# Kernel optimization log

Measured on AMD Instinct MI355X. Metric: run time of the kernel, lower is better.

The kernel has to match this reference:

```python
import jax, jax.numpy as jnp
import numpy as np

D_MODEL = 2048
N_HEADS = 16
N_KV_HEADS = 4
HEAD_DIM = D_MODEL // N_HEADS  # 128
N_REP = N_HEADS // N_KV_HEADS  # 4
ROPE_BASE = 10000.0


def _rope_tables(T, head_dim, dtype):
    inv_freq = 1.0 / (ROPE_BASE ** (jnp.arange(0, head_dim, 2, dtype=jnp.float32) / head_dim))
    t = jnp.arange(T, dtype=jnp.float32)
    freqs = jnp.outer(t, inv_freq)               # [T, hd/2]
    emb = jnp.concatenate([freqs, freqs], axis=-1)  # [T, hd]
    return jnp.cos(emb).astype(dtype), jnp.sin(emb).astype(dtype)


def _rotate_half(x):
    x1, x2 = jnp.split(x, 2, axis=-1)
    return jnp.concatenate([-x2, x1], axis=-1)


def _apply_rope(x, cos, sin):
    # x: [B, H, T, hd]; cos/sin: [T, hd]
    return x * cos[None, None] + _rotate_half(x) * sin[None, None]


def setup_inputs() -> dict:
    key = jax.random.key(0)
    ks = jax.random.split(key, 5)
    B, T = 2, 2048
    s_in = 1.0 / np.sqrt(D_MODEL)
    return {
        "x": jax.random.normal(ks[0], (B, T, D_MODEL), jnp.float32),
        "Wq": jax.random.normal(ks[1], (D_MODEL, D_MODEL), jnp.float32) * s_in,
        "Wk": jax.random.normal(ks[2], (D_MODEL, N_KV_HEADS * HEAD_DIM), jnp.float32) * s_in,
        "Wv": jax.random.normal(ks[3], (D_MODEL, N_KV_HEADS * HEAD_DIM), jnp.float32) * s_in,
        "Wo": jax.random.normal(ks[4], (D_MODEL, D_MODEL), jnp.float32) * s_in,
    }


def reference(x, Wq, Wk, Wv, Wo):
    B, T, C = x.shape
    scale = HEAD_DIM ** -0.5
    q = (x @ Wq).reshape(B, T, N_HEADS, HEAD_DIM).transpose(0, 2, 1, 3)     # [B,H,T,hd]
    k = (x @ Wk).reshape(B, T, N_KV_HEADS, HEAD_DIM).transpose(0, 2, 1, 3)  # [B,Hkv,T,hd]
    v = (x @ Wv).reshape(B, T, N_KV_HEADS, HEAD_DIM).transpose(0, 2, 1, 3)
    cos, sin = _rope_tables(T, HEAD_DIM, x.dtype)
    q = _apply_rope(q, cos, sin)
    k = _apply_rope(k, cos, sin)
    # GQA: group query heads; avoid materializing expanded K/V
    qg = q.reshape(B, N_KV_HEADS, N_REP, T, HEAD_DIM)
    scores = jnp.einsum('bgrtd,bgsd->bgrts', qg, k) * scale                 # [B,Hkv,rep,T,S]
    causal = jnp.tril(jnp.ones((T, T), dtype=bool))
    scores = jnp.where(causal[None, None, None], scores, jnp.finfo(scores.dtype).min)
    attn = jax.nn.softmax(scores, axis=-1)
    out = jnp.einsum('bgrts,bgsd->bgrtd', attn, v)                          # [B,Hkv,rep,T,hd]
    out = out.reshape(B, N_HEADS, T, HEAD_DIM).transpose(0, 2, 1, 3).reshape(B, T, C)
    return out @ Wo, k, v
```

## Files before the change

kernel.cpp:

```cpp
#include <hip/hip_runtime.h>
#include <hip/hip_bf16.h>
#include <type_traits>


typedef short  short8 __attribute__((ext_vector_type(8)));
typedef float  f32x4  __attribute__((ext_vector_type(4)));
typedef float  f32x16 __attribute__((ext_vector_type(16)));

#define AS1(p) ((__attribute__((address_space(1))) void*)(p))
#define AS3(p) ((__attribute__((address_space(3))) void*)(p))

static __device__ inline short bf_bits(float f) {
    __hip_bfloat16 h = __float2bfloat16(f);
    return *reinterpret_cast<short*>(&h);
}

__global__ __launch_bounds__(256) void convert_x_kernel(
    const float* __restrict__ x, __hip_bfloat16* __restrict__ xb)
{
    int i = (blockIdx.x * 256 + threadIdx.x) * 4;
    float4 v = *reinterpret_cast<const float4*>(x + i);
    ushort4 o;
    o.x = (unsigned short)bf_bits(v.x);
    o.y = (unsigned short)bf_bits(v.y);
    o.z = (unsigned short)bf_bits(v.z);
    o.w = (unsigned short)bf_bits(v.w);
    *reinterpret_cast<ushort4*>(reinterpret_cast<unsigned short*>(xb) + i) = o;
}

__global__ void transpose_all_kernel(
    const float* __restrict__ Wq, const float* __restrict__ Wk,
    const float* __restrict__ Wv, const float* __restrict__ Wo,
    __hip_bfloat16* __restrict__ WqkvT, __hip_bfloat16* __restrict__ WoT)
{
    __shared__ float tile[32][33];
    const int nb = blockIdx.x;
    const int k0 = blockIdx.y * 32;
    const int tx = threadIdx.x, ty = threadIdx.y;
    const float* W; int srcN, sn0, drow; __hip_bfloat16* dst;
    if (nb < 64) {
        int blk = nb & 3;
        int blk2 = ((blk & 1) << 1) | (blk >> 1);
        W = Wq; srcN = 2048; sn0 = nb * 32;
        dst = WqkvT; drow = ((nb >> 2) * 4 + blk2) * 32;
    } else if (nb < 80) {
        int i = nb - 64, blk = i & 3;
        int blk2 = ((blk & 1) << 1) | (blk >> 1);
        W = Wk; srcN = 512; sn0 = i * 32;
        dst = WqkvT; drow = 2048 + ((i >> 2) * 4 + blk2) * 32;
    } else if (nb < 96) {
        int i = nb - 80;
        W = Wv; srcN = 512; sn0 = i * 32;
        dst = WqkvT; drow = 2560 + i * 32;
    } else {
        int i = nb - 96;
        W = Wo; srcN = 2048; sn0 = i * 32;
        dst = WoT; drow = i * 32;
    }
#pragma unroll
    for (int i = 0; i < 32; i += 8)
        tile[ty + i][tx] = W[(size_t)(k0 + ty + i) * srcN + sn0 + tx];
    __syncthreads();
#pragma unroll
    for (int i = 0; i < 32; i += 8)
        dst[(size_t)(drow + ty + i) * 2048 + k0 + tx] = __float2bfloat16(tile[tx][ty + i]);
}

static __device__ inline void xcd_decode(int bid, int M, int N, int& m0, int& n0)
{
    const int xcd = bid & 7;
    const int idx = bid >> 3;
    const int mpx = (M >> 7) >> 3;
    const int rem = idx % (mpx * 4);
    const int mb = xcd * mpx + rem % mpx;
    const int nb = (idx / (mpx * 4)) * 4 + rem / mpx;
    m0 = mb << 7;
    n0 = nb << 7;
}

#define WAITV4 asm volatile("s_waitcnt vmcnt(4)" ::: "memory")
#define WAITV0 asm volatile("s_waitcnt vmcnt(0)" ::: "memory")

template <typename CT>
__global__ __launch_bounds__(256) void gemm_bt_kernel(
    const __hip_bfloat16* __restrict__ A,
    const __hip_bfloat16* __restrict__ BT,
    CT* __restrict__ C, int M, int N, int K)
{
    const int tid  = threadIdx.x;
    const int w    = tid >> 6;
    const int lane = tid & 63;
    const int l31  = lane & 31;
    const int hi   = lane >> 5;
    int m0, n0;
    xcd_decode(blockIdx.x, M, N, m0, n0);
    const int wm = (w >> 1) << 6;
    const int wn = (w & 1) << 6;

    __shared__ __hip_bfloat16 As[2][128 * 64];
    __shared__ __hip_bfloat16 Bs[2][128 * 64];

    f32x16 acc[2][2] = {};

#define GSTAGE(buf, k0_)                                                            \
    {                                                                               \
        _Pragma("unroll")                                                           \
        for (int i = 0; i < 4; ++i) {                                               \
            int c = tid + i * 256;                                                  \
            int row = c >> 3;                                                       \
            int soct = (c & 7) ^ (row & 7);                                         \
            const __hip_bfloat16* ga = A  + (size_t)(m0 + row) * K + (k0_) + soct * 8; \
            const __hip_bfloat16* gb = BT + (size_t)(n0 + row) * K + (k0_) + soct * 8; \
            __builtin_amdgcn_global_load_lds(AS1(ga), AS3(&As[buf][c * 8]), 16, 0, 0); \
            __builtin_amdgcn_global_load_lds(AS1(gb), AS3(&Bs[buf][c * 8]), 16, 0, 0); \
        }                                                                           \
    }

    GSTAGE(0, 0);
    __syncthreads();
    int cur = 0;
    const int nk = K >> 6;

    for (int t = 0; t < nk; ++t) {
        if (t + 1 < nk) GSTAGE(cur ^ 1, (t + 1) << 6);

#pragma unroll
        for (int ks = 0; ks < 4; ++ks) {
            const int oct = ((ks * 2 + hi) ^ (l31 & 7)) << 3;
            short8 a[2], b[2];
#pragma unroll
            for (int mi = 0; mi < 2; ++mi)
                a[mi] = *reinterpret_cast<const short8*>(
                    reinterpret_cast<const short*>(&As[cur][0]) + (wm + mi * 32 + l31) * 64 + oct);
#pragma unroll
            for (int ni = 0; ni < 2; ++ni)
                b[ni] = *reinterpret_cast<const short8*>(
                    reinterpret_cast<const short*>(&Bs[cur][0]) + (wn + ni * 32 + l31) * 64 + oct);
#pragma unroll
            for (int mi = 0; mi < 2; ++mi)
#pragma unroll
                for (int ni = 0; ni < 2; ++ni)
                    acc[mi][ni] = __builtin_amdgcn_mfma_f32_32x32x16_bf16(
                        a[mi], b[ni], acc[mi][ni], 0, 0, 0);
        }
        __syncthreads();
        cur ^= 1;
    }
#undef GSTAGE

#pragma unroll
    for (int mi = 0; mi < 2; ++mi)
#pragma unroll
        for (int ni = 0; ni < 2; ++ni)
#pragma unroll
            for (int reg = 0; reg < 16; ++reg) {
                int row = m0 + wm + mi * 32 + (reg & 3) + 8 * (reg >> 2) + 4 * hi;
                int col = n0 + wn + ni * 32 + l31;
                float v = acc[mi][ni][reg];
                if constexpr (std::is_same<CT, float>::value)
                    C[(size_t)row * N + col] = v;
                else
                    C[(size_t)row * N + col] = __float2bfloat16(v);
            }
}

__global__ __launch_bounds__(256) void gemm_qkv_fused(
    const __hip_bfloat16* __restrict__ A,
    const __hip_bfloat16* __restrict__ BT,
    __hip_bfloat16* __restrict__ qkv,
    float* __restrict__ outk,
    float* __restrict__ outv,
    __hip_bfloat16* __restrict__ VT)
{
    const int tid  = threadIdx.x;
    const int w    = tid >> 6;
    const int lane = tid & 63;
    const int l31  = lane & 31;
    const int hi   = lane >> 5;
    int m0, n0;
    xcd_decode(blockIdx.x, 4096, 3072, m0, n0);
    const int wm = (w >> 1) << 6;
    const int wn = (w & 1) << 6;
    const int K = 2048;

    __shared__ __hip_bfloat16 As[3][128 * 32];
    __shared__ __hip_bfloat16 Bs[3][128 * 32];

    f32x16 acc[2][2] = {};

#define GSTAGE(buf, k0_)                                                             \
    {                                                                                \
        _Pragma("unroll")                                                            \
        for (int i = 0; i < 2; ++i) {                                                \
            int c = tid + i * 256;                                                   \
            int row = c >> 2;                                                        \
            int soct = (c & 3) ^ ((row >> 1) & 3);                                   \
            const __hip_bfloat16* ga = A  + (size_t)(m0 + row) * K + (k0_) + soct * 8; \
            const __hip_bfloat16* gb = BT + (size_t)(n0 + row) * K + (k0_) + soct * 8; \
            __builtin_amdgcn_global_load_lds(AS1(ga), AS3(&As[buf][c * 8]), 16, 0, 0); \
            __builtin_amdgcn_global_load_lds(AS1(gb), AS3(&Bs[buf][c * 8]), 16, 0, 0); \
        }                                                                            \
    }

    const int nk = 64;
    GSTAGE(0, 0);
    GSTAGE(1, 32);
    int cur = 0, stg = 2;

    for (int t = 0; t < nk; ++t) {
        if (t == nk - 1) { WAITV0; } else { WAITV4; }
        __builtin_amdgcn_s_barrier();
        __builtin_amdgcn_sched_barrier(0);
        if (t + 2 < nk) GSTAGE(stg, (t + 2) << 5);

#pragma unroll
        for (int ks = 0; ks < 2; ++ks) {
            short8 a[2], b[2];
#pragma unroll
            for (int mi = 0; mi < 2; ++mi) {
                int row = wm + mi * 32 + l31;
                a[mi] = *reinterpret_cast<const short8*>(
                    reinterpret_cast<const short*>(&As[cur][0])
                    + row * 32 + (((ks * 2 + hi) ^ ((row >> 1) & 3)) << 3));
            }
#pragma unroll
            for (int ni = 0; ni < 2; ++ni) {
                int row = wn + ni * 32 + l31;
                b[ni] = *reinterpret_cast<const short8*>(
                    reinterpret_cast<const short*>(&Bs[cur][0])
                    + row * 32 + (((ks * 2 + hi) ^ ((row >> 1) & 3)) << 3));
            }
#pragma unroll
            for (int mi = 0; mi < 2; ++mi)
#pragma unroll
                for (int ni = 0; ni < 2; ++ni)
                    acc[mi][ni] = __builtin_amdgcn_mfma_f32_32x32x16_bf16(
                        a[mi], b[ni], acc[mi][ni], 0, 0, 0);
        }
        cur = (cur == 2) ? 0 : cur + 1;
        stg = (stg == 2) ? 0 : stg + 1;
    }
#undef GSTAGE

    const int hc = n0 >> 7;
    if (hc < 20) {
        const int c0 = wn + l31;
        const int d_lo = (wn ? 32 : 0) + l31;
        const float invf = exp2f((float)d_lo * -0.20762050593046f);
        const int kh = hc - 16;
#pragma unroll
        for (int mi = 0; mi < 2; ++mi)
#pragma unroll
            for (int reg = 0; reg < 16; ++reg) {
                int row = m0 + wm + mi * 32 + (reg & 3) + 8 * (reg >> 2) + 4 * hi;
                int b = row >> 11, t = row & 2047;
                float ang = (float)t * invf;
                float s = __sinf(ang), c = __cosf(ang);
                float x1 = acc[mi][0][reg], x2 = acc[mi][1][reg];
                float o1 = x1 * c - x2 * s;
                float o2 = x2 * c + x1 * s;
                __hip_bfloat16* q = qkv + (size_t)row * 3072 + hc * 128 + c0;
                q[0]  = __float2bfloat16(o1);
                q[32] = __float2bfloat16(o2);
                if (hc >= 16) {
                    float* ok = outk + (size_t)((b * 4 + kh) * 2048 + t) * 128 + d_lo;
                    ok[0]  = o1;
                    ok[64] = o2;
                }
            }
    } else {
        const int kh = hc - 20;
#pragma unroll
        for (int mi = 0; mi < 2; ++mi)
#pragma unroll
            for (int reg = 0; reg < 16; ++reg) {
                int row = m0 + wm + mi * 32 + (reg & 3) + 8 * (reg >> 2) + 4 * hi;
                int b = row >> 11, t = row & 2047;
#pragma unroll
                for (int ni = 0; ni < 2; ++ni) {
                    int d = wn + ni * 32 + l31;
                    float v = acc[mi][ni][reg];
                    outv[(size_t)((b * 4 + kh) * 2048 + t) * 128 + d] = v;
                    VT[(size_t)((b * 4 + kh) * 128 + d) * 2048 + t] = __float2bfloat16(v);
                }
            }
    }
}

__global__ __launch_bounds__(256, 2) void attn_kernel(
    const __hip_bfloat16* __restrict__ qkv,
    const __hip_bfloat16* __restrict__ VT,
    __hip_bfloat16* __restrict__ outO)
{
    const int bh = blockIdx.x;
    const int b = bh >> 4, h = bh & 15;
    const int kh = h >> 2;
    const int yb = blockIdx.y;
    const int qblk = (yb < 8) ? (15 - yb) : (yb - 8);
    const int tid = threadIdx.x;
    const int w = tid >> 6;
    const int lane = tid & 63;
    const int lo16 = lane & 15, grp = lane >> 4;
    const int qrow0 = qblk * 128 + w * 32;

    __shared__ short Ks[2][64 * 128];
    __shared__ short Vs[2][128 * 64];
    __shared__ short Ps[4][32 * 64];

    const short* qkvs = reinterpret_cast<const short*>(qkv);
    const size_t kbase = (size_t)b * 2048 * 3072 + 2048 + kh * 128;
    const short* vtb = reinterpret_cast<const short*>(VT) + (size_t)(b * 4 + kh) * 128 * 2048;
    short* pw = &Ps[w][0];

    short8 qf[2][4];
#pragma unroll
    for (int mi = 0; mi < 2; ++mi) {
        const short* qp = qkvs + (size_t)(b * 2048 + qrow0 + mi * 16 + lo16) * 3072
                        + h * 128 + grp * 8;
#pragma unroll
        for (int ss = 0; ss < 4; ++ss)
            qf[mi][ss] = *reinterpret_cast<const short8*>(qp + ss * 32);
    }

    f32x4 o[2][8] = {};
    f32x4 lac[2] = {};

    short8 ones;
#pragma unroll
    for (int jj = 0; jj < 8; ++jj) ones[jj] = (short)0x3F80;

    const float scl2 = 0.12752749545902973f;
    const int ntiles = qblk * 2 + 2;

#define STAGE(buf, kb_)                                                              \
    {                                                                                \
        _Pragma("unroll")                                                            \
        for (int i = 0; i < 4; ++i) {                                                \
            int c = tid + i * 256;                                                   \
            int row = c >> 4, c16 = (c & 15) ^ (row & 7);                            \
            const short* src = qkvs + kbase + (size_t)((kb_) + row) * 3072 + c16 * 8;\
            __builtin_amdgcn_global_load_lds(AS1(src),                               \
                AS3(&Ks[buf][(w * 64 + i * 256) * 8]), 16, 0, 0);                    \
        }                                                                            \
        _Pragma("unroll")                                                            \
        for (int i = 0; i < 4; ++i) {                                                \
            int c = tid + i * 256;                                                   \
            int d = c >> 3, c8 = (c & 7) ^ (d & 7);                                  \
            const short* src = vtb + (size_t)d * 2048 + (kb_) + c8 * 8;              \
            __builtin_amdgcn_global_load_lds(AS1(src),                               \
                AS3(&Vs[buf][(w * 64 + i * 256) * 8]), 16, 0, 0);                    \
        }                                                                            \
    }

    STAGE(0, 0);
    __syncthreads();
    int cur = 0;

    for (int t = 0; t < ntiles; ++t) {
        const int kb = t * 64;
        if (t + 1 < ntiles) STAGE(cur ^ 1, kb + 64);

        f32x4 sg[2][4];
        __builtin_amdgcn_s_setprio(1);
#pragma unroll
        for (int kg = 0; kg < 4; ++kg) {
            f32x4 a0 = {}, a1 = {};
#pragma unroll
            for (int ss = 0; ss < 4; ++ss) {
                short8 kf = *reinterpret_cast<const short8*>(
                    &Ks[cur][(kg * 16 + lo16) * 128 + (((ss * 4 + grp) ^ (lo16 & 7)) << 3)]);
                a0 = __builtin_amdgcn_mfma_f32_16x16x32_bf16(qf[0][ss], kf, a0, 0, 0, 0);
                a1 = __builtin_amdgcn_mfma_f32_16x16x32_bf16(qf[1][ss], kf, a1, 0, 0, 0);
            }
            sg[0][kg] = a0; sg[1][kg] = a1;
        }
        __builtin_amdgcn_s_setprio(0);

        if (kb + 63 > qrow0) {
#pragma unroll
            for (int mi = 0; mi < 2; ++mi)
#pragma unroll
                for (int kg = 0; kg < 4; ++kg) {
                    const int key = kb + kg * 16 + lo16;
#pragma unroll
                    for (int r = 0; r < 4; ++r) {
                        float v = sg[mi][kg][r] * scl2;
                        sg[mi][kg][r] = (key <= qrow0 + mi * 16 + grp * 4 + r) ? v : -1e30f;
                    }
                }
        } else {
#pragma unroll
            for (int mi = 0; mi < 2; ++mi)
#pragma unroll
                for (int kg = 0; kg < 4; ++kg)
#pragma unroll
                    for (int r = 0; r < 4; ++r) sg[mi][kg][r] *= scl2;
        }

#pragma unroll
        for (int mi = 0; mi < 2; ++mi)
#pragma unroll
            for (int kg = 0; kg < 4; ++kg)
#pragma unroll
                for (int r = 0; r < 4; ++r) {
                    float p = __builtin_amdgcn_exp2f(sg[mi][kg][r]);
                    int row = mi * 16 + grp * 4 + r;
                    int idx = row * 64 + (((kg * 2 + (lo16 >> 3)) ^ (row & 7)) << 3) + (lo16 & 7);
                    pw[idx] = bf_bits(p);
                }

        __builtin_amdgcn_s_setprio(1);
#pragma unroll
        for (int ks = 0; ks < 2; ++ks) {
            short8 pf0 = *reinterpret_cast<const short8*>(
                &pw[(0 * 16 + lo16) * 64 + (((ks * 4 + grp) ^ (lo16 & 7)) << 3)]);
            short8 pf1 = *reinterpret_cast<const short8*>(
                &pw[(1 * 16 + lo16) * 64 + (((ks * 4 + grp) ^ (lo16 & 7)) << 3)]);
            lac[0] = __builtin_amdgcn_mfma_f32_16x16x32_bf16(pf0, ones, lac[0], 0, 0, 0);
            lac[1] = __builtin_amdgcn_mfma_f32_16x16x32_bf16(pf1, ones, lac[1], 0, 0, 0);
#pragma unroll
            for (int jj = 0; jj < 8; ++jj) {
                short8 vf = *reinterpret_cast<const short8*>(
                    &Vs[cur][(jj * 16 + lo16) * 64 + (((ks * 4 + grp) ^ (lo16 & 7)) << 3)]);
                o[0][jj] = __builtin_amdgcn_mfma_f32_16x16x32_bf16(pf0, vf, o[0][jj], 0, 0, 0);
                o[1][jj] = __builtin_amdgcn_mfma_f32_16x16x32_bf16(pf1, vf, o[1][jj], 0, 0, 0);
            }
        }
        __builtin_amdgcn_s_setprio(0);

        __syncthreads();
        cur ^= 1;
    }
#undef STAGE

#pragma unroll
    for (int mi = 0; mi < 2; ++mi)
#pragma unroll
        for (int r = 0; r < 4; ++r) {
            float inv = 1.0f / lac[mi][r];
#pragma unroll
            for (int jj = 0; jj < 8; ++jj) {
                outO[(size_t)(b * 2048 + qrow0 + mi * 16 + grp * 4 + r) * 2048
                     + h * 128 + jj * 16 + lo16] = __float2bfloat16(o[mi][jj][r] * inv);
            }
        }
}

extern "C" void kernel_launch(void* const* d_in, const int* in_sizes, int n_in,
                              void* d_out, int out_size, void* d_ws, size_t ws_size,
                              hipStream_t stream)
{
    (void)in_sizes; (void)n_in; (void)out_size; (void)ws_size;
    const float* x  = (const float*)d_in[0];
    const float* Wq = (const float*)d_in[1];
    const float* Wk = (const float*)d_in[2];
    const float* Wv = (const float*)d_in[3];
    const float* Wo = (const float*)d_in[4];

    float* out0 = (float*)d_out;
    float* outk = out0 + 8388608;
    float* outv = out0 + 10485760;

    __hip_bfloat16* wsb    = (__hip_bfloat16*)d_ws;
    __hip_bfloat16* xb     = wsb;
    __hip_bfloat16* WqkvT  = xb + 8388608;
    __hip_bfloat16* WoT    = WqkvT + 6291456;
    __hip_bfloat16* qkv    = WoT + 4194304;
    __hip_bfloat16* VT     = qkv + 12582912;
    __hip_bfloat16* attn_o = xb;

    convert_x_kernel<<<8192, 256, 0, stream>>>(x, xb);
    transpose_all_kernel<<<dim3(160, 64), dim3(32, 8), 0, stream>>>(
        Wq, Wk, Wv, Wo, WqkvT, WoT);

    gemm_qkv_fused<<<768, 256, 0, stream>>>(xb, WqkvT, qkv, outk, outv, VT);

    attn_kernel<<<dim3(32, 16), 256, 0, stream>>>(qkv, VT, attn_o);

    gemm_bt_kernel<float><<<512, 256, 0, stream>>>(attn_o, WoT, out0, 4096, 2048, 2048);
}
```

Baseline: 190.8 us.

## Retile QKV GEMM to 256x256 with 512 threads and merge prep kernels

The QKV projection GEMM moves from 128x128 tiles with 256 threads and triple buffering to 256x256 tiles with 8 waves and a 4-stage LDS pipeline. The epilogue indexing is adjusted so each wave's 128-column half still maps to one head for RoPE and the K/V writes. Larger tiles raise operand reuse per LDS load, but each block now needs about 128KB of LDS, which limits it to one block per CU. The grid also shrinks to 192 blocks, fewer than the CU count, so some CUs sit idle. Separately, the x-to-bf16 conversion and the weight-transpose kernels are merged into one launch to remove a kernel boundary.

```diff
diff --git a/kernel.cpp b/kernel.cpp
--- a/kernel.cpp
+++ b/kernel.cpp
@@ -15,28 +15,29 @@
     return *reinterpret_cast<short*>(&h);
 }
 
-__global__ __launch_bounds__(256) void convert_x_kernel(
-    const float* __restrict__ x, __hip_bfloat16* __restrict__ xb)
-{
-    int i = (blockIdx.x * 256 + threadIdx.x) * 4;
-    float4 v = *reinterpret_cast<const float4*>(x + i);
-    ushort4 o;
-    o.x = (unsigned short)bf_bits(v.x);
-    o.y = (unsigned short)bf_bits(v.y);
-    o.z = (unsigned short)bf_bits(v.z);
-    o.w = (unsigned short)bf_bits(v.w);
-    *reinterpret_cast<ushort4*>(reinterpret_cast<unsigned short*>(xb) + i) = o;
-}
-
-__global__ void transpose_all_kernel(
+__global__ void prep_kernel(
+    const float* __restrict__ x,
     const float* __restrict__ Wq, const float* __restrict__ Wk,
     const float* __restrict__ Wv, const float* __restrict__ Wo,
+    __hip_bfloat16* __restrict__ xb,
     __hip_bfloat16* __restrict__ WqkvT, __hip_bfloat16* __restrict__ WoT)
 {
+    const int nb = blockIdx.x;
+    const int tx = threadIdx.x, ty = threadIdx.y;
+    if (nb >= 160) {
+        int bid2 = (nb - 160) * 64 + blockIdx.y;
+        int i = (bid2 * 256 + ty * 32 + tx) * 4;
+        float4 v = *reinterpret_cast<const float4*>(x + i);
+        ushort4 o;
+        o.x = (unsigned short)bf_bits(v.x);
+        o.y = (unsigned short)bf_bits(v.y);
+        o.z = (unsigned short)bf_bits(v.z);
+        o.w = (unsigned short)bf_bits(v.w);
+        *reinterpret_cast<ushort4*>(reinterpret_cast<unsigned short*>(xb) + i) = o;
+        return;
+    }
     __shared__ float tile[32][33];
-    const int nb = blockIdx.x;
     const int k0 = blockIdx.y * 32;
-    const int tx = threadIdx.x, ty = threadIdx.y;
     const float* W; int srcN, sn0, drow; __hip_bfloat16* dst;
     if (nb < 64) {
         int blk = nb & 3;
@@ -78,6 +79,7 @@
     n0 = nb << 7;
 }
 
+#define WAITV8 asm volatile("s_waitcnt vmcnt(8)" ::: "memory")
 #define WAITV4 asm volatile("s_waitcnt vmcnt(4)" ::: "memory")
 #define WAITV0 asm volatile("s_waitcnt vmcnt(0)" ::: "memory")
 
@@ -164,7 +166,7 @@
             }
 }
 
-__global__ __launch_bounds__(256) void gemm_qkv_fused(
+__global__ __launch_bounds__(512, 2) void gemm_qkv_fused(
     const __hip_bfloat16* __restrict__ A,
     const __hip_bfloat16* __restrict__ BT,
     __hip_bfloat16* __restrict__ qkv,
@@ -177,22 +179,25 @@
     const int lane = tid & 63;
     const int l31  = lane & 31;
     const int hi   = lane >> 5;
-    int m0, n0;
-    xcd_decode(blockIdx.x, 4096, 3072, m0, n0);
-    const int wm = (w >> 1) << 6;
-    const int wn = (w & 1) << 6;
+    const int bid  = blockIdx.x;
+    const int xcd  = bid & 7;
+    const int idx  = bid >> 3;
+    const int m0   = (xcd * 2 + (idx & 1)) << 8;
+    const int n0   = (idx >> 1) << 8;
+    const int wm   = (w >> 2) << 7;
+    const int wn   = (w & 3) << 6;
     const int K = 2048;
 
-    __shared__ __hip_bfloat16 As[3][128 * 32];
-    __shared__ __hip_bfloat16 Bs[3][128 * 32];
-
-    f32x16 acc[2][2] = {};
+    __shared__ __hip_bfloat16 As[4][256 * 32];
+    __shared__ __hip_bfloat16 Bs[4][256 * 32];
+
+    f32x16 acc[4][2] = {};
 
 #define GSTAGE(buf, k0_)                                                             \
     {                                                                                \
         _Pragma("unroll")                                                            \
         for (int i = 0; i < 2; ++i) {                                                \
-            int c = tid + i * 256;                                                   \
+            int c = tid + i * 512;                                                   \
             int row = c >> 2;                                                        \
             int soct = (c & 3) ^ ((row >> 1) & 3);                                   \
             const __hip_bfloat16* ga = A  + (size_t)(m0 + row) * K + (k0_) + soct * 8; \
@@ -205,19 +210,22 @@
     const int nk = 64;
     GSTAGE(0, 0);
     GSTAGE(1, 32);
-    int cur = 0, stg = 2;
+    GSTAGE(2, 64);
+    int cur = 0, stg = 3;
 
     for (int t = 0; t < nk; ++t) {
-        if (t == nk - 1) { WAITV0; } else { WAITV4; }
+        if (t < nk - 2)      { WAITV8; }
+        else if (t == nk - 2) { WAITV4; }
+        else                  { WAITV0; }
         __builtin_amdgcn_s_barrier();
         __builtin_amdgcn_sched_barrier(0);
-        if (t + 2 < nk) GSTAGE(stg, (t + 2) << 5);
+        if (t + 3 < nk) GSTAGE(stg, (t + 3) << 5);
 
 #pragma unroll
         for (int ks = 0; ks < 2; ++ks) {
-            short8 a[2], b[2];
-#pragma unroll
-            for (int mi = 0; mi < 2; ++mi) {
+            short8 a[4], b[2];
+#pragma unroll
+            for (int mi = 0; mi < 4; ++mi) {
                 int row = wm + mi * 32 + l31;
                 a[mi] = *reinterpret_cast<const short8*>(
                     reinterpret_cast<const short*>(&As[cur][0])
@@ -231,25 +239,25 @@
                     + row * 32 + (((ks * 2 + hi) ^ ((row >> 1) & 3)) << 3));
             }
 #pragma unroll
-            for (int mi = 0; mi < 2; ++mi)
+            for (int mi = 0; mi < 4; ++mi)
 #pragma unroll
                 for (int ni = 0; ni < 2; ++ni)
                     acc[mi][ni] = __builtin_amdgcn_mfma_f32_32x32x16_bf16(
                         a[mi], b[ni], acc[mi][ni], 0, 0, 0);
         }
-        cur = (cur == 2) ? 0 : cur + 1;
-        stg = (stg == 2) ? 0 : stg + 1;
+        cur = (cur + 1) & 3;
+        stg = (stg + 1) & 3;
     }
 #undef GSTAGE
 
-    const int hc = n0 >> 7;
+    const int hc = (n0 >> 7) + (wn >> 7);
     if (hc < 20) {
-        const int c0 = wn + l31;
-        const int d_lo = (wn ? 32 : 0) + l31;
+        const int c0 = (wn & 64) + l31;
+        const int d_lo = ((wn & 64) >> 1) + l31;
         const float invf = exp2f((float)d_lo * -0.20762050593046f);
         const int kh = hc - 16;
 #pragma unroll
-        for (int mi = 0; mi < 2; ++mi)
+        for (int mi = 0; mi < 4; ++mi)
 #pragma unroll
             for (int reg = 0; reg < 16; ++reg) {
                 int row = m0 + wm + mi * 32 + (reg & 3) + 8 * (reg >> 2) + 4 * hi;
@@ -271,14 +279,14 @@
     } else {
         const int kh = hc - 20;
 #pragma unroll
-        for (int mi = 0; mi < 2; ++mi)
+        for (int mi = 0; mi < 4; ++mi)
 #pragma unroll
             for (int reg = 0; reg < 16; ++reg) {
                 int row = m0 + wm + mi * 32 + (reg & 3) + 8 * (reg >> 2) + 4 * hi;
                 int b = row >> 11, t = row & 2047;
 #pragma unroll
                 for (int ni = 0; ni < 2; ++ni) {
-                    int d = wn + ni * 32 + l31;
+                    int d = (wn & 64) + ni * 32 + l31;
                     float v = acc[mi][ni][reg];
                     outv[(size_t)((b * 4 + kh) * 2048 + t) * 128 + d] = v;
                     VT[(size_t)((b * 4 + kh) * 128 + d) * 2048 + t] = __float2bfloat16(v);
@@ -469,11 +477,10 @@
     __hip_bfloat16* VT     = qkv + 12582912;
     __hip_bfloat16* attn_o = xb;
 
-    convert_x_kernel<<<8192, 256, 0, stream>>>(x, xb);
-    transpose_all_kernel<<<dim3(160, 64), dim3(32, 8), 0, stream>>>(
-        Wq, Wk, Wv, Wo, WqkvT, WoT);
-
-    gemm_qkv_fused<<<768, 256, 0, stream>>>(xb, WqkvT, qkv, outk, outv, VT);
+    prep_kernel<<<dim3(288, 64), dim3(32, 8), 0, stream>>>(
+        x, Wq, Wk, Wv, Wo, xb, WqkvT, WoT);
+
+    gemm_qkv_fused<<<192, 512, 0, stream>>>(xb, WqkvT, qkv, outk, outv, VT);
 
     attn_kernel<<<dim3(32, 16), 256, 0, stream>>>(qkv, VT, attn_o);
 
```

New measurement: 208.7 us. +9.3%, slower.

## Split heavy causal attention blocks across KV halves and merge partials; fuse prep kernels

Applied to the files above, without the earlier changes.

Query blocks 8-15 now have their KV tile range split into two halves, each processed by a separate workgroup. Unnormalized partial outputs and row sums go to scratch in the output buffer, and a new merge kernel combines them. This balances the causal triangular workload over 768 blocks instead of 512 uneven ones. The bf16 conversion of x is folded into the weight transpose launch to remove one kernel launch. The cost is an extra merge launch and partial-output traffic, and partial O is rounded to bf16 before the merge.

```diff
diff --git a/kernel.cpp b/kernel.cpp
--- a/kernel.cpp
+++ b/kernel.cpp
@@ -15,28 +15,29 @@
     return *reinterpret_cast<short*>(&h);
 }
 
-__global__ __launch_bounds__(256) void convert_x_kernel(
-    const float* __restrict__ x, __hip_bfloat16* __restrict__ xb)
-{
-    int i = (blockIdx.x * 256 + threadIdx.x) * 4;
-    float4 v = *reinterpret_cast<const float4*>(x + i);
-    ushort4 o;
-    o.x = (unsigned short)bf_bits(v.x);
-    o.y = (unsigned short)bf_bits(v.y);
-    o.z = (unsigned short)bf_bits(v.z);
-    o.w = (unsigned short)bf_bits(v.w);
-    *reinterpret_cast<ushort4*>(reinterpret_cast<unsigned short*>(xb) + i) = o;
-}
-
-__global__ void transpose_all_kernel(
+__global__ void prep_kernel(
+    const float* __restrict__ x,
     const float* __restrict__ Wq, const float* __restrict__ Wk,
     const float* __restrict__ Wv, const float* __restrict__ Wo,
+    __hip_bfloat16* __restrict__ xb,
     __hip_bfloat16* __restrict__ WqkvT, __hip_bfloat16* __restrict__ WoT)
 {
+    const int nb = blockIdx.x;
+    const int tx = threadIdx.x, ty = threadIdx.y;
+    if (nb >= 160) {
+        int bid2 = (nb - 160) * 64 + blockIdx.y;
+        int i = (bid2 * 256 + ty * 32 + tx) * 4;
+        float4 v = *reinterpret_cast<const float4*>(x + i);
+        ushort4 o;
+        o.x = (unsigned short)bf_bits(v.x);
+        o.y = (unsigned short)bf_bits(v.y);
+        o.z = (unsigned short)bf_bits(v.z);
+        o.w = (unsigned short)bf_bits(v.w);
+        *reinterpret_cast<ushort4*>(reinterpret_cast<unsigned short*>(xb) + i) = o;
+        return;
+    }
     __shared__ float tile[32][33];
-    const int nb = blockIdx.x;
     const int k0 = blockIdx.y * 32;
-    const int tx = threadIdx.x, ty = threadIdx.y;
     const float* W; int srcN, sn0, drow; __hip_bfloat16* dst;
     if (nb < 64) {
         int blk = nb & 3;
@@ -290,13 +291,25 @@
 __global__ __launch_bounds__(256, 2) void attn_kernel(
     const __hip_bfloat16* __restrict__ qkv,
     const __hip_bfloat16* __restrict__ VT,
-    __hip_bfloat16* __restrict__ outO)
-{
-    const int bh = blockIdx.x;
+    __hip_bfloat16* __restrict__ outO,
+    __hip_bfloat16* __restrict__ o_part,
+    float* __restrict__ l_part)
+{
+    const int bid = blockIdx.x;
+    const int bh = bid & 31;
+    const int s = bid >> 5;
+    int qblk, half = 0, t0, t1;
+    bool split;
+    if (s < 8) {
+        qblk = s; split = false;
+        t0 = 0; t1 = 2 * s + 2;
+    } else {
+        qblk = 8 + ((s - 8) >> 1); half = (s - 8) & 1; split = true;
+        int nt = 2 * qblk + 2, mid = qblk + 1;
+        t0 = half ? mid : 0; t1 = half ? nt : mid;
+    }
     const int b = bh >> 4, h = bh & 15;
     const int kh = h >> 2;
-    const int yb = blockIdx.y;
-    const int qblk = (yb < 8) ? (15 - yb) : (yb - 8);
     const int tid = threadIdx.x;
     const int w = tid >> 6;
     const int lane = tid & 63;
@@ -330,7 +343,6 @@
     for (int jj = 0; jj < 8; ++jj) ones[jj] = (short)0x3F80;
 
     const float scl2 = 0.12752749545902973f;
-    const int ntiles = qblk * 2 + 2;
 
 #define STAGE(buf, kb_)                                                              \
     {                                                                                \
@@ -352,13 +364,13 @@
         }                                                                            \
     }
 
-    STAGE(0, 0);
+    STAGE(0, t0 * 64);
     __syncthreads();
     int cur = 0;
 
-    for (int t = 0; t < ntiles; ++t) {
+    for (int t = t0; t < t1; ++t) {
         const int kb = t * 64;
-        if (t + 1 < ntiles) STAGE(cur ^ 1, kb + 64);
+        if (t + 1 < t1) STAGE(cur ^ 1, kb + 64);
 
         f32x4 sg[2][4];
         __builtin_amdgcn_s_setprio(1);
@@ -433,17 +445,63 @@
     }
 #undef STAGE
 
-#pragma unroll
-    for (int mi = 0; mi < 2; ++mi)
-#pragma unroll
-        for (int r = 0; r < 4; ++r) {
-            float inv = 1.0f / lac[mi][r];
-#pragma unroll
-            for (int jj = 0; jj < 8; ++jj) {
-                outO[(size_t)(b * 2048 + qrow0 + mi * 16 + grp * 4 + r) * 2048
-                     + h * 128 + jj * 16 + lo16] = __float2bfloat16(o[mi][jj][r] * inv);
-            }
-        }
+    if (!split) {
+#pragma unroll
+        for (int mi = 0; mi < 2; ++mi)
+#pragma unroll
+            for (int r = 0; r < 4; ++r) {
+                float inv = 1.0f / lac[mi][r];
+#pragma unroll
+                for (int jj = 0; jj < 8; ++jj) {
+                    outO[(size_t)(b * 2048 + qrow0 + mi * 16 + grp * 4 + r) * 2048
+                         + h * 128 + jj * 16 + lo16] = __float2bfloat16(o[mi][jj][r] * inv);
+                }
+            }
+    } else {
+        const int hq = qblk - 8;
+        const size_t pbase = (((size_t)bh * 8 + hq) * 2 + half) * 128;
+#pragma unroll
+        for (int mi = 0; mi < 2; ++mi)
+#pragma unroll
+            for (int r = 0; r < 4; ++r) {
+                int pr = w * 32 + mi * 16 + grp * 4 + r;
+#pragma unroll
+                for (int jj = 0; jj < 8; ++jj)
+                    o_part[(pbase + pr) * 128 + jj * 16 + lo16] =
+                        __float2bfloat16(o[mi][jj][r]);
+                if (lo16 == 0) l_part[pbase + pr] = lac[mi][r];
+            }
+    }
+}
+
+__global__ __launch_bounds__(256) void attn_merge_kernel(
+    const __hip_bfloat16* __restrict__ o_part,
+    const float* __restrict__ l_part,
+    __hip_bfloat16* __restrict__ outO)
+{
+    int idx = blockIdx.x * 256 + threadIdx.x;
+    int d4 = (idx & 31) * 4;
+    int pr = (idx >> 5) & 127;
+    int hq = (idx >> 12) & 7;
+    int bh = idx >> 15;
+    size_t pb = (((size_t)bh * 8 + hq) * 2) * 128 + pr;
+    const ushort4 u0 = *reinterpret_cast<const ushort4*>(
+        reinterpret_cast<const unsigned short*>(o_part) + pb * 128 + d4);
+    const ushort4 u1 = *reinterpret_cast<const ushort4*>(
+        reinterpret_cast<const unsigned short*>(o_part) + (pb + 128) * 128 + d4);
+    float l = l_part[pb] + l_part[pb + 128];
+    float inv = 1.0f / l;
+    int b = bh >> 4, h = bh & 15;
+    int row = (8 + hq) * 128 + pr;
+    __hip_bfloat16* dst = outO + (size_t)(b * 2048 + row) * 2048 + h * 128 + d4;
+    unsigned short us[4] = {u0.x, u0.y, u0.z, u0.w};
+    unsigned short vs[4] = {u1.x, u1.y, u1.z, u1.w};
+#pragma unroll
+    for (int j = 0; j < 4; ++j) {
+        float a = __bfloat162float(*reinterpret_cast<__hip_bfloat16*>(&us[j]));
+        float c = __bfloat162float(*reinterpret_cast<__hip_bfloat16*>(&vs[j]));
+        dst[j] = __float2bfloat16((a + c) * inv);
+    }
 }
 
 extern "C" void kernel_launch(void* const* d_in, const int* in_sizes, int n_in,
@@ -460,6 +518,9 @@
     float* out0 = (float*)d_out;
     float* outk = out0 + 8388608;
     float* outv = out0 + 10485760;
+
+    __hip_bfloat16* o_part = (__hip_bfloat16*)out0;
+    float* l_part = out0 + 4194304;
 
     __hip_bfloat16* wsb    = (__hip_bfloat16*)d_ws;
     __hip_bfloat16* xb     = wsb;
@@ -469,13 +530,13 @@
     __hip_bfloat16* VT     = qkv + 12582912;
     __hip_bfloat16* attn_o = xb;
 
-    convert_x_kernel<<<8192, 256, 0, stream>>>(x, xb);
-    transpose_all_kernel<<<dim3(160, 64), dim3(32, 8), 0, stream>>>(
-        Wq, Wk, Wv, Wo, WqkvT, WoT);
+    prep_kernel<<<dim3(288, 64), dim3(32, 8), 0, stream>>>(
+        x, Wq, Wk, Wv, Wo, xb, WqkvT, WoT);
 
     gemm_qkv_fused<<<768, 256, 0, stream>>>(xb, WqkvT, qkv, outk, outv, VT);
 
-    attn_kernel<<<dim3(32, 16), 256, 0, stream>>>(qkv, VT, attn_o);
+    attn_kernel<<<768, 256, 0, stream>>>(qkv, VT, attn_o, o_part, l_part);
+    attn_merge_kernel<<<4096, 256, 0, stream>>>(o_part, l_part, attn_o);
 
     gemm_bt_kernel<float><<<512, 256, 0, stream>>>(attn_o, WoT, out0, 4096, 2048, 2048);
 }
```

Result: slower. 200.6 us (+5.1%).
